# Kernel optimization log

Hardware: AMD Instinct MI355X
Metric: run time of the kernel (lower is better)

Reference implementation:

```python
import jax, jax.numpy as jnp
import numpy as np

EPS = np.finfo(np.float32).eps
X_DIM, H_DIM, Z_DIM = 256, 1024, 128
T, B = 128, 256

def _lin(key, fan_in, fan_out):
    k1, k2 = jax.random.split(key)
    lim = 1.0 / np.sqrt(fan_in)
    W = jax.random.uniform(k1, (fan_in, fan_out), jnp.float32, -lim, lim)
    b = jax.random.uniform(k2, (fan_out,), jnp.float32, -lim, lim)
    return W, b

def setup_inputs() -> dict:
    key = jax.random.key(0)
    ks = jax.random.split(key, 20)
    inp = {}
    inp['x'] = jax.random.normal(ks[0], (T, B, X_DIM), jnp.float32)
    inp['h'] = jnp.zeros((1, B, H_DIM), jnp.float32)
    inp['eps'] = jax.random.normal(ks[1], (T, B, Z_DIM), jnp.float32)
    inp['Wpx'], inp['bpx'] = _lin(ks[2], X_DIM, H_DIM)
    inp['Wpz'], inp['bpz'] = _lin(ks[3], Z_DIM, H_DIM)
    inp['Wenc'], inp['benc'] = _lin(ks[4], 2 * H_DIM, H_DIM)
    inp['Wem'], inp['bem'] = _lin(ks[5], H_DIM, Z_DIM)
    inp['Wes'], inp['bes'] = _lin(ks[6], H_DIM, Z_DIM)
    inp['Wpr'], inp['bpr'] = _lin(ks[7], H_DIM, H_DIM)
    inp['Wpm'], inp['bpm'] = _lin(ks[8], H_DIM, Z_DIM)
    inp['Wps'], inp['bps'] = _lin(ks[9], H_DIM, Z_DIM)
    inp['Wdec'], inp['bdec'] = _lin(ks[10], 2 * H_DIM, H_DIM)
    inp['Wdm'], inp['bdm'] = _lin(ks[11], H_DIM, X_DIM)
    inp['Wds'], inp['bds'] = _lin(ks[12], H_DIM, X_DIM)
    # GRU (pytorch layout): W_ih [3H, 2H], W_hh [3H, H]
    lim = 1.0 / np.sqrt(H_DIM)
    inp['W_ih'] = jax.random.uniform(ks[13], (3 * H_DIM, 2 * H_DIM), jnp.float32, -lim, lim)
    inp['W_hh'] = jax.random.uniform(ks[14], (3 * H_DIM, H_DIM), jnp.float32, -lim, lim)
    inp['b_ih'] = jax.random.uniform(ks[15], (3 * H_DIM,), jnp.float32, -lim, lim)
    inp['b_hh'] = jax.random.uniform(ks[16], (3 * H_DIM,), jnp.float32, -lim, lim)
    return inp

def reference(x, h, eps, Wpx, bpx, Wpz, bpz, Wenc, benc, Wem, bem, Wes, bes,
              Wpr, bpr, Wpm, bpm, Wps, bps, Wdec, bdec, Wdm, bdm, Wds, bds,
              W_ih, W_hh, b_ih, b_hh):
    relu = jax.nn.relu
    sp = jax.nn.softplus

    def gru_cell(inp, h_prev):
        gi = inp @ W_ih.T + b_ih          # [B, 3H]
        gh = h_prev @ W_hh.T + b_hh       # [B, 3H]
        i_r, i_z, i_n = jnp.split(gi, 3, axis=-1)
        h_r, h_z, h_n = jnp.split(gh, 3, axis=-1)
        r = jax.nn.sigmoid(i_r + h_r)
        u = jax.nn.sigmoid(i_z + h_z)
        n = jnp.tanh(i_n + r * h_n)
        return (1.0 - u) * n + u * h_prev

    def step(h_t, xe):
        x_t, eps_t = xe
        phi_x_t = relu(x_t @ Wpx + bpx)                               # [B,H]
        enc_t = relu(jnp.concatenate([phi_x_t, h_t], axis=1) @ Wenc + benc)
        enc_mean_t = enc_t @ Wem + bem
        enc_std_t = sp(enc_t @ Wes + bes)
        z_t = enc_mean_t + eps_t * enc_std_t                          # reparam
        phi_z_t = relu(z_t @ Wpz + bpz)
        prior_t = relu(h_t @ Wpr + bpr)
        prior_mean_t = prior_t @ Wpm + bpm
        prior_std_t = sp(prior_t @ Wps + bps)
        dec_t = relu(jnp.concatenate([phi_z_t, h_t], axis=1) @ Wdec + bdec)
        dec_mean_t = dec_t @ Wdm + bdm
        dec_std_t = sp(dec_t @ Wds + bds)
        h_next = gru_cell(jnp.concatenate([phi_x_t, phi_z_t], axis=1), h_t)
        kld_t = 0.5 * jnp.sum(2.0 * jnp.log(prior_std_t + EPS) - 2.0 * jnp.log(enc_std_t + EPS)
                              + (enc_std_t ** 2 + (enc_mean_t - prior_mean_t) ** 2) / prior_std_t ** 2 - 1.0)
        nll_t = jnp.sum(jnp.log(dec_std_t + EPS) + 0.5 * jnp.log(2.0 * jnp.pi)
                        + (x_t - dec_mean_t) ** 2 / (2.0 * dec_std_t ** 2))
        return h_next, (enc_mean_t, enc_std_t, dec_mean_t, dec_std_t, kld_t, nll_t)

    h0 = h[0]  # [B, H]
    _, (enc_means, enc_stds, dec_means, dec_stds, klds, nlls) = jax.lax.scan(step, h0, (x, eps))
    kld_loss = jnp.sum(klds)
    nll_loss = jnp.sum(nlls)
    return (kld_loss, nll_loss, enc_means, enc_stds, dec_means, dec_stds)
```

## Files before the change

### kernel.cpp

```cpp
#include <hip/hip_runtime.h>
#include <math.h>
#include <limits.h>

#define T_DIM 128
#define B_DIM 256
#define X_DIMC 256
#define H_DIMC 1024
#define Z_DIMC 128
#define EPSF 1.1920929e-07f
#define HALF_LOG_2PI 0.91893853320467274f
#define NBLK 768
#define NPB (NBLK / 64)
#define BARN ((66 + 64) * 32)

typedef float f32x4 __attribute__((ext_vector_type(4)));
typedef short bf16x8 __attribute__((ext_vector_type(8)));

struct Seg { int n_end; int kbeg; int kend; const float* bias; int act;
             float* of32; int ld32; short* ob16; int ld16; };
struct Segs { Seg s[4]; };

__host__ __device__ static inline Seg dseg(int n_end, int kbeg, int kend,
    const float* bias, int act, float* of32, int ld32, short* ob16, int ld16)
{
    Seg s; s.n_end = n_end; s.kbeg = kbeg; s.kend = kend; s.bias = bias;
    s.act = act; s.of32 = of32; s.ld32 = ld32; s.ob16 = ob16; s.ld16 = ld16;
    return s;
}
__host__ __device__ static inline Seg dsegend()
{ return dseg(INT_MAX, 0, 64, nullptr, 0, nullptr, 0, nullptr, 0); }

__device__ __forceinline__ short f2bf(float f) {
    unsigned u = __builtin_bit_cast(unsigned, f);
    u += 0x7fffu + ((u >> 16) & 1u);
    return (short)(u >> 16);
}
__device__ __forceinline__ float act_apply(float x, int act) {
    if (act == 1) return fmaxf(x, 0.f);
    if (act == 2) return x > 0.f ? x + log1pf(expf(-x)) : log1pf(expf(x));
    return x;
}
__device__ __forceinline__ void gload16(const short* g, short* l) {
    __builtin_amdgcn_global_load_lds(
        (const __attribute__((address_space(1))) void*)g,
        (__attribute__((address_space(3))) void*)l, 16, 0, 0);
}
__device__ __forceinline__ void gload16a(const short* g, short* l) {
    __builtin_amdgcn_global_load_lds(
        (const __attribute__((address_space(1))) void*)g,
        (__attribute__((address_space(3))) void*)l, 16, 0, 17);
}
__device__ __forceinline__ float ldf(const float* p) {
    return __hip_atomic_load(p, __ATOMIC_RELAXED, __HIP_MEMORY_SCOPE_AGENT);
}
__device__ __forceinline__ void stf(float* p, float v) {
    __hip_atomic_store(p, v, __ATOMIC_RELAXED, __HIP_MEMORY_SCOPE_AGENT);
}
__device__ __forceinline__ void sth(short* p, short v) {
    __hip_atomic_store(p, v, __ATOMIC_RELAXED, __HIP_MEMORY_SCOPE_AGENT);
}

__device__ __forceinline__ void gridbar(unsigned* bar, int phase) {
    __syncthreads();
    if (threadIdx.x == 0) {
        asm volatile("s_waitcnt vmcnt(0) lgkmcnt(0)" ::: "memory");
        const int leaf = blockIdx.x & 63;
        unsigned* leafc = bar + (leaf << 5);
        unsigned* rootc = bar + (64 << 5);
        unsigned* rgen  = bar + (65 << 5);
        unsigned* lgen  = bar + ((66 + leaf) << 5);
        unsigned old = __hip_atomic_fetch_add(leafc, 1u, __ATOMIC_RELAXED,
                                              __HIP_MEMORY_SCOPE_AGENT);
        if (((old + 1u) % (unsigned)NPB) == 0u) {
            unsigned r = __hip_atomic_fetch_add(rootc, 1u, __ATOMIC_RELAXED,
                                                __HIP_MEMORY_SCOPE_AGENT);
            if (((r + 1u) & 63u) == 0u)
                __hip_atomic_store(rgen, (r + 1u) >> 6, __ATOMIC_RELAXED,
                                   __HIP_MEMORY_SCOPE_AGENT);
            unsigned g; int it = 0;
            while ((int)(g = __hip_atomic_load(rgen, __ATOMIC_RELAXED,
                                               __HIP_MEMORY_SCOPE_AGENT)) < phase) {
                if (it < 4) { __builtin_amdgcn_s_sleep(1); ++it; }
                else        { __builtin_amdgcn_s_sleep(8); }
            }
            __hip_atomic_store(lgen, g, __ATOMIC_RELAXED,
                               __HIP_MEMORY_SCOPE_AGENT);
        } else {
            int it = 0;
            while ((int)__hip_atomic_load(lgen, __ATOMIC_RELAXED,
                                          __HIP_MEMORY_SCOPE_AGENT) < phase) {
                if (it < 4) { __builtin_amdgcn_s_sleep(1); ++it; }
                else        { __builtin_amdgcn_s_sleep(8); }
            }
        }
    }
    __syncthreads();
}

__device__ __forceinline__ void gemm_tile(
    short* __restrict__ smem, int bm0, int bn0,
    const short* __restrict__ A0, int lda0,
    const short* __restrict__ A1, int lda1,
    const short* __restrict__ A2, int lda2,
    int ks1, int ks2, int a0c,
    const short* __restrict__ BT, int ldb, const Segs& segs)
{
    short* As = smem;
    short* Bs = smem + 12288;
    const int tid = threadIdx.x, lane = tid & 63, wid = tid >> 6;
    __syncthreads();
    Seg sg; int n0;
    if      (bn0 < segs.s[0].n_end) { sg = segs.s[0]; n0 = 0; }
    else if (bn0 < segs.s[1].n_end) { sg = segs.s[1]; n0 = segs.s[0].n_end; }
    else if (bn0 < segs.s[2].n_end) { sg = segs.s[2]; n0 = segs.s[1].n_end; }
    else                            { sg = segs.s[3]; n0 = segs.s[2].n_end; }
    const int nit = (sg.kend - sg.kbeg) >> 5;
    const int row16 = lane >> 2;
    const int kc = ((lane & 3) ^ ((lane >> 3) & 3)) << 3;
    const int r0 = (wid << 4) + row16;

    auto srcA = [&](int gk) -> const short* {
        return (gk < ks1) ? A0 + (size_t)(bm0 + r0) * lda0 + gk
             : (gk < ks2) ? A1 + (size_t)(bm0 + r0) * lda1 + (gk - ks1)
                          : A2 + (size_t)(bm0 + r0) * lda2 + (gk - ks2);
    };
    auto stage = [&](int p, int it) {
        const int gk = sg.kbeg + (it << 5) + kc;
        short* dA = As + p * 2048 + (wid << 9);
        short* dB = Bs + p * 2048 + (wid << 9);
        const short* ga = srcA(gk);
        if (a0c && gk < ks1) gload16(ga, dA);
        else                 gload16a(ga, dA);
        gload16(BT + (size_t)(bn0 + r0) * ldb + gk, dB);
    };

    const int l15 = lane & 15, lg = lane >> 4;
    const int wm = (wid >> 1) << 5, wn = (wid & 1) << 5;
    const int co = (lg ^ ((l15 >> 1) & 3)) << 3;
    f32x4 acc[2][2] = {};

#pragma unroll
    for (int i = 0; i < 6; ++i) if (i < nit) stage(i, i);
    int p = 0;
    for (int it = 0; it < nit; ++it) {
        const int rem = nit - 1 - it;
        if      (rem >= 5) asm volatile("s_waitcnt vmcnt(10)" ::: "memory");
        else if (rem == 4) asm volatile("s_waitcnt vmcnt(8)" ::: "memory");
        else if (rem == 3) asm volatile("s_waitcnt vmcnt(6)" ::: "memory");
        else if (rem == 2) asm volatile("s_waitcnt vmcnt(4)" ::: "memory");
        else if (rem == 1) asm volatile("s_waitcnt vmcnt(2)" ::: "memory");
        else               asm volatile("s_waitcnt vmcnt(0)" ::: "memory");
        asm volatile("s_barrier" ::: "memory");
        const short* Ap = As + p * 2048;
        const short* Bp = Bs + p * 2048;
        bf16x8 a0 = *(const bf16x8*)(Ap + (wm + l15) * 32 + co);
        bf16x8 a1 = *(const bf16x8*)(Ap + (wm + 16 + l15) * 32 + co);
        bf16x8 b0 = *(const bf16x8*)(Bp + (wn + l15) * 32 + co);
        bf16x8 b1 = *(const bf16x8*)(Bp + (wn + 16 + l15) * 32 + co);
        acc[0][0] = __builtin_amdgcn_mfma_f32_16x16x32_bf16(a0, b0, acc[0][0], 0, 0, 0);
        acc[0][1] = __builtin_amdgcn_mfma_f32_16x16x32_bf16(a0, b1, acc[0][1], 0, 0, 0);
        acc[1][0] = __builtin_amdgcn_mfma_f32_16x16x32_bf16(a1, b0, acc[1][0], 0, 0, 0);
        acc[1][1] = __builtin_amdgcn_mfma_f32_16x16x32_bf16(a1, b1, acc[1][1], 0, 0, 0);
        if (rem >= 6) {
            asm volatile("s_waitcnt lgkmcnt(0)\n\ts_barrier" ::: "memory");
            stage(p, it + 6);
        }
        p = (p == 5) ? 0 : p + 1;
    }

#pragma unroll
    for (int j = 0; j < 2; ++j) {
        const int gn = bn0 + wn + (j << 4) + l15;
        const int cn = gn - n0;
        const float bv = sg.bias[cn];
#pragma unroll
        for (int i = 0; i < 2; ++i) {
            const int gm0 = bm0 + wm + (i << 4) + (lg << 2);
#pragma unroll
            for (int r = 0; r < 4; ++r) {
                float v = act_apply(acc[i][j][r] + bv, sg.act);
                if (sg.of32) stf(sg.of32 + (size_t)(gm0 + r) * sg.ld32 + cn, v);
                if (sg.ob16) sth(sg.ob16 + (size_t)(gm0 + r) * sg.ld16 + cn, f2bf(v));
            }
        }
    }
}

__device__ __forceinline__ void z_tile(
    short* __restrict__ smem, int bm0, int bn0,
    const float* __restrict__ zm, const float* __restrict__ zs,
    const float* __restrict__ ze,
    const short* __restrict__ BT, const float* __restrict__ bias,
    short* __restrict__ outb)
{
    short* Az = smem;
    short* Bz = smem + 64 * 136;
    const int tid = threadIdx.x, lane = tid & 63, wid = tid >> 6;
    __syncthreads();
    const int r = tid >> 2, c0i = (tid & 3) << 3;
#pragma unroll
    for (int s = 0; s < 4; ++s) {
        const int col = c0i + s * 32;
        const size_t base = (size_t)(bm0 + r) * 128 + col;
        short tmp[8];
#pragma unroll
        for (int q = 0; q < 8; ++q) {
            const float m = ldf(zm + base + q);
            const float sd = ldf(zs + base + q);
            const float e = ze[base + q];
            tmp[q] = f2bf(fmaf(e, sd, m));
        }
        *(bf16x8*)(Az + r * 136 + col) = *(bf16x8*)tmp;
        *(bf16x8*)(Bz + r * 136 + col) =
            *(const bf16x8*)(BT + (size_t)(bn0 + r) * 128 + col);
    }
    __syncthreads();
    const int l15 = lane & 15, lg = lane >> 4;
    const int wm = (wid >> 1) << 5, wn = (wid & 1) << 5;
    f32x4 acc[2][2] = {};
#pragma unroll
    for (int s = 0; s < 4; ++s) {
        bf16x8 af0 = *(const bf16x8*)(Az + (wm + l15) * 136 + (lg << 3) + s * 32);
        bf16x8 af1 = *(const bf16x8*)(Az + (wm + 16 + l15) * 136 + (lg << 3) + s * 32);
        bf16x8 bg0 = *(const bf16x8*)(Bz + (wn + l15) * 136 + (lg << 3) + s * 32);
        bf16x8 bg1 = *(const bf16x8*)(Bz + (wn + 16 + l15) * 136 + (lg << 3) + s * 32);
        acc[0][0] = __builtin_amdgcn_mfma_f32_16x16x32_bf16(af0, bg0, acc[0][0], 0, 0, 0);
        acc[0][1] = __builtin_amdgcn_mfma_f32_16x16x32_bf16(af0, bg1, acc[0][1], 0, 0, 0);
        acc[1][0] = __builtin_amdgcn_mfma_f32_16x16x32_bf16(af1, bg0, acc[1][0], 0, 0, 0);
        acc[1][1] = __builtin_amdgcn_mfma_f32_16x16x32_bf16(af1, bg1, acc[1][1], 0, 0, 0);
    }
#pragma unroll
    for (int j = 0; j < 2; ++j) {
        const int gn = bn0 + wn + (j << 4) + l15;
        const float bv = bias[gn];
#pragma unroll
        for (int i = 0; i < 2; ++i) {
            const int gm0 = bm0 + wm + (i << 4) + (lg << 2);
#pragma unroll
            for (int rr = 0; rr < 4; ++rr) {
                float v = fmaxf(acc[i][j][rr] + bv, 0.f);
                sth(outb + (size_t)(gm0 + rr) * 1024 + gn, f2bf(v));
            }
        }
    }
}

__device__ __forceinline__ void gru_unit(int uid, int tid,
    const float* __restrict__ gi, const float* __restrict__ gh,
    const float* __restrict__ h, float* __restrict__ hn, short* __restrict__ hnb)
{
    const int i = uid * 256 + tid;
    const int b = i >> 10, j = i & (H_DIMC - 1);
    const float* gib = gi + (size_t)b * 3 * H_DIMC;
    const float* ghb = gh + (size_t)b * 3 * H_DIMC;
    const float r = 1.f / (1.f + expf(-(ldf(gib + j) + ldf(ghb + j))));
    const float u = 1.f / (1.f + expf(-(ldf(gib + H_DIMC + j) + ldf(ghb + H_DIMC + j))));
    const float n = tanhf(ldf(gib + 2 * H_DIMC + j) + r * ldf(ghb + 2 * H_DIMC + j));
    const float v = (1.f - u) * n + u * ldf(h + i);
    stf(hn + i, v); sth(hnb + i, f2bf(v));
}

__device__ __forceinline__ void loss_unit(int uid, int tid,
    const float* __restrict__ em, const float* __restrict__ es,
    const float* __restrict__ pm, const float* __restrict__ ps,
    const float* __restrict__ xt, const float* __restrict__ dm,
    const float* __restrict__ ds, float* __restrict__ outp, float* sred)
{
    const int KB = (B_DIM * Z_DIMC) / 256;
    float v; int target;
    if (uid < KB) {
        const int i = uid * 256 + tid;
        const float esv = ldf(es + i), psv = ldf(ps + i);
        const float dmn = ldf(em + i) - ldf(pm + i);
        v = 0.5f * (2.f * logf(psv + EPSF) - 2.f * logf(esv + EPSF) +
                    (esv * esv + dmn * dmn) / (psv * psv) - 1.f);
        target = 0;
    } else {
        const int i = (uid - KB) * 256 + tid;
        const float d = ldf(ds + i);
        const float diff = xt[i] - ldf(dm + i);
        v = logf(d + EPSF) + HALF_LOG_2PI + diff * diff / (2.f * d * d);
        target = 1;
    }
    for (int o = 32; o > 0; o >>= 1) v += __shfl_down(v, o);
    if ((tid & 63) == 0) sred[tid >> 6] = v;
    __syncthreads();
    if (tid == 0) atomicAdd(outp + target, sred[0] + sred[1] + sred[2] + sred[3]);
    __syncthreads();
}

struct PP {
    const short* xb; const float* x; const float* eps;
    const short *WTpx, *WT1, *WT2, *WTpz, *WT4, *WT56;
    const float *bpx, *benc, *bpr, *bhh, *bem, *bes, *bpz, *bdec, *bih,
                *bpm, *bps, *bdm, *bds;
    float *hf0, *hf1; short *hb0, *hb1;
    short *enc_b, *prior_b, *phi_zb, *dec_b;
    short *phiXb, *phiXs;
    float *ghb, *gib, *pmb, *psb;
    float *kld, *em, *es, *dm, *ds;
    unsigned* bar; int big;
};

__global__ __launch_bounds__(256, 3) void vrnn_k(PP p)
{
    __shared__ short smem[24576];
    __shared__ float sred[4];
    const int G = gridDim.x, bid = blockIdx.x, tid = threadIdx.x;
    const int BIGK = 1 << 30;
    int ph = 0;

    Segs sx;
    sx.s[0] = dseg(1024, 0, 256, p.bpx, 1, nullptr, 0, p.big ? p.phiXb : p.phiXs, 1024);
    sx.s[1] = dsegend(); sx.s[2] = dsegend(); sx.s[3] = dsegend();

    if (p.big) {
        for (int u = bid; u < 512 * 16; u += G)
            gemm_tile(smem, (u & 511) << 6, (u >> 9) << 6,
                      p.xb, 256, p.xb, 256, p.xb, 256, BIGK, BIGK, 1,
                      p.WTpx, 256, sx);
        gridbar(p.bar, ++ph);
    }

    for (int t = 0; t < T_DIM; ++t) {
        float* hcur = (t & 1) ? p.hf1 : p.hf0;
        float* hnxt = (t & 1) ? p.hf0 : p.hf1;
        const short* hbc = (t & 1) ? p.hb1 : p.hb0;
        short* hbn = (t & 1) ? p.hb0 : p.hb1;
        const short* phiXt = p.big ? p.phiXb + (size_t)t * B_DIM * H_DIMC : p.phiXs;
        float* em_t = p.em + (size_t)t * B_DIM * Z_DIMC;
        float* es_t = p.es + (size_t)t * B_DIM * Z_DIMC;
        float* dm_t = p.dm + (size_t)t * B_DIM * X_DIMC;
        float* ds_t = p.ds + (size_t)t * B_DIM * X_DIMC;
        const float* eps_t = p.eps + (size_t)t * B_DIM * Z_DIMC;

        if (!p.big) {
            for (int u = bid; u < 64; u += G)
                gemm_tile(smem, (u & 3) << 6, (u >> 2) << 6,
                          p.xb + (size_t)t * B_DIM * X_DIMC, 256,
                          p.xb, 256, p.xb, 256, BIGK, BIGK, 1, p.WTpx, 256, sx);
            gridbar(p.bar, ++ph);
        }
        {
            Segs g1;
            g1.s[0] = dseg(1024, 0, 2048, p.benc, 1, nullptr, 0, p.enc_b, 1024);
            g1.s[1] = dseg(2048, 1024, 2048, p.bpr, 1, nullptr, 0, p.prior_b, 1024);
            g1.s[2] = dseg(5120, 1024, 2048, p.bhh, 0, p.ghb, 3 * H_DIMC, nullptr, 0);
            g1.s[3] = dsegend();
            const int tp = t - 1;
            const int nA = 320 + (t > 0 ? 384 : 0);
            for (int u = bid; u < nA; u += G) {
                if (u < 320)
                    gemm_tile(smem, (u & 3) << 6, (u >> 2) << 6,
                              phiXt, 1024, hbc, 1024, hbc, 1024, 1024, BIGK, 1,
                              p.WT1, 2048, g1);
                else
                    loss_unit(u - 320, tid,
                              p.em + (size_t)tp * B_DIM * Z_DIMC,
                              p.es + (size_t)tp * B_DIM * Z_DIMC,
                              p.pmb, p.psb,
                              p.x + (size_t)tp * B_DIM * X_DIMC,
                              p.dm + (size_t)tp * B_DIM * X_DIMC,
                              p.ds + (size_t)tp * B_DIM * X_DIMC,
                              p.kld, sred);
            }
            gridbar(p.bar, ++ph);
        }
        {
            Segs g2;
            g2.s[0] = dseg(128, 0, 1024, p.bem, 0, em_t, 128, nullptr, 0);
            g2.s[1] = dseg(256, 0, 1024, p.bes, 2, es_t, 128, nullptr, 0);
            g2.s[2] = dsegend(); g2.s[3] = dsegend();
            for (int u = bid; u < 16; u += G)
                gemm_tile(smem, (u & 3) << 6, (u >> 2) << 6,
                          p.enc_b, 1024, p.enc_b, 1024, p.enc_b, 1024, BIGK, BIGK, 0,
                          p.WT2, 1024, g2);
            gridbar(p.bar, ++ph);
        }
        for (int u = bid; u < 64; u += G)
            z_tile(smem, (u & 3) << 6, (u >> 2) << 6,
                   em_t, es_t, eps_t, p.WTpz, p.bpz, p.phi_zb);
        gridbar(p.bar, ++ph);
        {
            Segs g4;
            g4.s[0] = dseg(1024, 1024, 3072, p.bdec, 1, nullptr, 0, p.dec_b, 1024);
            g4.s[1] = dseg(4096, 0, 2048, p.bih, 0, p.gib, 3 * H_DIMC, nullptr, 0);
            g4.s[2] = dsegend(); g4.s[3] = dsegend();
            for (int u = bid; u < 256; u += G)
                gemm_tile(smem, (u & 3) << 6, (u >> 2) << 6,
                          phiXt, 1024, p.phi_zb, 1024, hbc, 1024, 1024, 2048, 1,
                          p.WT4, 3072, g4);
            gridbar(p.bar, ++ph);
        }
        {
            Segs g5;
            g5.s[0] = dseg(128, 0, 1024, p.bpm, 0, p.pmb, 128, nullptr, 0);
            g5.s[1] = dseg(256, 0, 1024, p.bps, 2, p.psb, 128, nullptr, 0);
            g5.s[2] = dseg(512, 1024, 2048, p.bdm, 0, dm_t, 256, nullptr, 0);
            g5.s[3] = dseg(768, 1024, 2048, p.bds, 2, ds_t, 256, nullptr, 0);
            for (int u = bid; u < 48 + 1024; u += G) {
                if (u < 48)
                    gemm_tile(smem, (u & 3) << 6, (u >> 2) << 6,
                              p.prior_b, 1024, p.dec_b, 1024, p.dec_b, 1024,
                              1024, BIGK, 0, p.WT56, 2048, g5);
                else
                    gru_unit(u - 48, tid, p.gib, p.ghb, hcur, hnxt, hbn);
            }
            gridbar(p.bar, ++ph);
        }
    }
    {
        const int tp = T_DIM - 1;
        for (int u = bid; u < 384; u += G)
            loss_unit(u, tid,
                      p.em + (size_t)tp * B_DIM * Z_DIMC,
                      p.es + (size_t)tp * B_DIM * Z_DIMC,
                      p.pmb, p.psb,
                      p.x + (size_t)tp * B_DIM * X_DIMC,
                      p.dm + (size_t)tp * B_DIM * X_DIMC,
                      p.ds + (size_t)tp * B_DIM * X_DIMC,
                      p.kld, sred);
    }
}

__global__ void packT_k(const float* __restrict__ src, int ldsr,
                        short* __restrict__ dst, int ldd, int n0, int k0)
{
    __shared__ float tile[32][33];
    const int bx = blockIdx.x * 32, by = blockIdx.y * 32;
    const int tx = threadIdx.x, ty = threadIdx.y;
    for (int i = ty; i < 32; i += 8)
        tile[i][tx] = src[(size_t)(by + i) * ldsr + bx + tx];
    __syncthreads();
    for (int i = ty; i < 32; i += 8)
        dst[(size_t)(n0 + bx + i) * ldd + k0 + by + tx] = f2bf(tile[tx][i]);
}

__global__ void packD_k(const float* __restrict__ src, int ldsr,
                        short* __restrict__ dst, int ldd, int n0, int k0, int kr)
{
    const int idx = blockIdx.x * 256 + threadIdx.x;
    const int n = idx / kr, k = idx % kr;
    dst[(size_t)(n0 + n) * ldd + k0 + k] = f2bf(src[(size_t)n * ldsr + k]);
}

__global__ void cvtx_k(const float* __restrict__ x, short* __restrict__ xb)
{
    const int i = blockIdx.x * 256 + threadIdx.x;
    float4 v = ((const float4*)x)[i];
    short4 s;
    s.x = f2bf(v.x); s.y = f2bf(v.y); s.z = f2bf(v.z); s.w = f2bf(v.w);
    ((short4*)xb)[i] = s;
}

__global__ void hinit_k(const float* __restrict__ h0, float* __restrict__ hf,
                        short* __restrict__ hb)
{
    const int i = blockIdx.x * 256 + threadIdx.x;
    const float v = h0[i];
    hf[i] = v; hb[i] = f2bf(v);
}

__global__ void init_k(unsigned* bar, float* kn)
{
    for (int i = threadIdx.x; i < BARN; i += 256) bar[i] = 0u;
    if (threadIdx.x < 2) kn[threadIdx.x] = 0.f;
}

extern "C" void kernel_launch(void* const* d_in, const int* in_sizes, int n_in,
                              void* d_out_v, int out_size, void* d_ws, size_t ws_size,
                              hipStream_t stream)
{
    (void)in_sizes; (void)n_in; (void)out_size;
    const float* x    = (const float*)d_in[0];
    const float* h0   = (const float*)d_in[1];
    const float* eps  = (const float*)d_in[2];
    const float* Wpx  = (const float*)d_in[3];
    const float* bpx  = (const float*)d_in[4];
    const float* Wpz  = (const float*)d_in[5];
    const float* bpz  = (const float*)d_in[6];
    const float* Wenc = (const float*)d_in[7];
    const float* benc = (const float*)d_in[8];
    const float* Wem  = (const float*)d_in[9];
    const float* bem  = (const float*)d_in[10];
    const float* Wes  = (const float*)d_in[11];
    const float* bes  = (const float*)d_in[12];
    const float* Wpr  = (const float*)d_in[13];
    const float* bpr  = (const float*)d_in[14];
    const float* Wpm  = (const float*)d_in[15];
    const float* bpm  = (const float*)d_in[16];
    const float* Wps  = (const float*)d_in[17];
    const float* bps  = (const float*)d_in[18];
    const float* Wdec = (const float*)d_in[19];
    const float* bdec = (const float*)d_in[20];
    const float* Wdm  = (const float*)d_in[21];
    const float* bdm  = (const float*)d_in[22];
    const float* Wds  = (const float*)d_in[23];
    const float* bds  = (const float*)d_in[24];
    const float* W_ih = (const float*)d_in[25];
    const float* W_hh = (const float*)d_in[26];
    const float* b_ih = (const float*)d_in[27];
    const float* b_hh = (const float*)d_in[28];

    float* out = (float*)d_out_v;

    char* wsb = (char*)d_ws;
    size_t off = 0;
    auto takeB = [&](size_t bytes) {
        char* p = wsb + off; off += (bytes + 255) & ~(size_t)255; return p;
    };
    short* WTpx = (short*)takeB((size_t)1024 * 256 * 2);
    short* WT1  = (short*)takeB((size_t)5120 * 2048 * 2);
    short* WT2  = (short*)takeB((size_t)256 * 1024 * 2);
    short* WTpz = (short*)takeB((size_t)1024 * 128 * 2);
    short* WT4  = (short*)takeB((size_t)4096 * 3072 * 2);
    short* WT56 = (short*)takeB((size_t)768 * 2048 * 2);
    short* xb   = (short*)takeB((size_t)T_DIM * B_DIM * X_DIMC * 2);
    float* hf0  = (float*)takeB((size_t)B_DIM * H_DIMC * 4);
    float* hf1  = (float*)takeB((size_t)B_DIM * H_DIMC * 4);
    short* hb0  = (short*)takeB((size_t)B_DIM * H_DIMC * 2);
    short* hb1  = (short*)takeB((size_t)B_DIM * H_DIMC * 2);
    short* enc_b   = (short*)takeB((size_t)B_DIM * H_DIMC * 2);
    short* prior_b = (short*)takeB((size_t)B_DIM * H_DIMC * 2);
    short* phi_zb  = (short*)takeB((size_t)B_DIM * H_DIMC * 2);
    short* dec_b   = (short*)takeB((size_t)B_DIM * H_DIMC * 2);
    float* ghb_ = (float*)takeB((size_t)B_DIM * 3 * H_DIMC * 4);
    float* gib_ = (float*)takeB((size_t)B_DIM * 3 * H_DIMC * 4);
    float* pmb  = (float*)takeB((size_t)B_DIM * Z_DIMC * 4);
    float* psb  = (float*)takeB((size_t)B_DIM * Z_DIMC * 4);
    unsigned* bar = (unsigned*)takeB((size_t)BARN * 4);
    const size_t phiXb_bytes = (size_t)T_DIM * B_DIM * H_DIMC * 2;
    const bool big = (off + phiXb_bytes) <= ws_size;
    short* phiXb = big ? (short*)takeB(phiXb_bytes) : nullptr;
    short* phiXs = big ? nullptr : (short*)takeB((size_t)B_DIM * H_DIMC * 2);

    const dim3 tb(256), pt(32, 8);

    packT_k<<<dim3(32, 8), pt, 0, stream>>>(Wpx, 1024, WTpx, 256, 0, 0);
    packT_k<<<dim3(32, 64), pt, 0, stream>>>(Wenc, 1024, WT1, 2048, 0, 0);
    packT_k<<<dim3(32, 32), pt, 0, stream>>>(Wpr, 1024, WT1, 2048, 1024, 1024);
    packD_k<<<dim3(3072 * 1024 / 256), tb, 0, stream>>>(W_hh, 1024, WT1, 2048, 2048, 1024, 1024);
    packT_k<<<dim3(4, 32), pt, 0, stream>>>(Wem, 128, WT2, 1024, 0, 0);
    packT_k<<<dim3(4, 32), pt, 0, stream>>>(Wes, 128, WT2, 1024, 128, 0);
    packT_k<<<dim3(32, 4), pt, 0, stream>>>(Wpz, 1024, WTpz, 128, 0, 0);
    packT_k<<<dim3(32, 64), pt, 0, stream>>>(Wdec, 1024, WT4, 3072, 0, 1024);
    packD_k<<<dim3(3072 * 2048 / 256), tb, 0, stream>>>(W_ih, 2048, WT4, 3072, 1024, 0, 2048);
    packT_k<<<dim3(4, 32), pt, 0, stream>>>(Wpm, 128, WT56, 2048, 0, 0);
    packT_k<<<dim3(4, 32), pt, 0, stream>>>(Wps, 128, WT56, 2048, 128, 0);
    packT_k<<<dim3(8, 32), pt, 0, stream>>>(Wdm, 256, WT56, 2048, 256, 1024);
    packT_k<<<dim3(8, 32), pt, 0, stream>>>(Wds, 256, WT56, 2048, 512, 1024);

    cvtx_k<<<dim3((size_t)T_DIM * B_DIM * X_DIMC / 4 / 256), tb, 0, stream>>>(x, xb);
    hinit_k<<<dim3(B_DIM * H_DIMC / 256), tb, 0, stream>>>(h0, hf0, hb0);
    init_k<<<1, 256, 0, stream>>>(bar, out);

    PP p;
    p.xb = xb; p.x = x; p.eps = eps;
    p.WTpx = WTpx; p.WT1 = WT1; p.WT2 = WT2; p.WTpz = WTpz; p.WT4 = WT4; p.WT56 = WT56;
    p.bpx = bpx; p.benc = benc; p.bpr = bpr; p.bhh = b_hh; p.bem = bem; p.bes = bes;
    p.bpz = bpz; p.bdec = bdec; p.bih = b_ih; p.bpm = bpm; p.bps = bps;
    p.bdm = bdm; p.bds = bds;
    p.hf0 = hf0; p.hf1 = hf1; p.hb0 = hb0; p.hb1 = hb1;
    p.enc_b = enc_b; p.prior_b = prior_b; p.phi_zb = phi_zb; p.dec_b = dec_b;
    p.phiXb = phiXb; p.phiXs = phiXs;
    p.ghb = ghb_; p.gib = gib_; p.pmb = pmb; p.psb = psb;
    p.kld = out; p.em = out + 2;
    p.es = p.em + (size_t)T_DIM * B_DIM * Z_DIMC;
    p.dm = p.es + (size_t)T_DIM * B_DIM * Z_DIMC;
    p.ds = p.dm + (size_t)T_DIM * B_DIM * X_DIMC;
    p.bar = bar; p.big = big ? 1 : 0;

    vrnn_k<<<dim3(NBLK), tb, 0, stream>>>(p);
}
```

Baseline: 15.27 ms.

## Split persistent grid into two independent batch-half groups with separate barriers

Splits the 768-block persistent kernel into two groups of 384 blocks. Each group handles 128 batch rows and syncs on its own hierarchical grid barrier. Because the batch rows are independent through the recurrence, each barrier now waits on half as many blocks, which should cut barrier latency per phase. The cost is half the tiles per group per phase, so small GEMM phases leave even more blocks idle, and weight reads are duplicated across the groups.

Result: faster. 14.71 ms (-3.7%).

```diff
diff --git a/kernel.cpp b/kernel.cpp
--- a/kernel.cpp
+++ b/kernel.cpp
@@ -10,7 +10,8 @@
 #define EPSF 1.1920929e-07f
 #define HALF_LOG_2PI 0.91893853320467274f
 #define NBLK 768
-#define NPB (NBLK / 64)
+#define GBLK 384
+#define NPB (GBLK / 64)
 #define BARN ((66 + 64) * 32)
 
 typedef float f32x4 __attribute__((ext_vector_type(4)));
@@ -60,11 +61,11 @@
     __hip_atomic_store(p, v, __ATOMIC_RELAXED, __HIP_MEMORY_SCOPE_AGENT);
 }
 
-__device__ __forceinline__ void gridbar(unsigned* bar, int phase) {
+__device__ __forceinline__ void gridbar(unsigned* bar, int phase, int lbid) {
     __syncthreads();
     if (threadIdx.x == 0) {
         asm volatile("s_waitcnt vmcnt(0) lgkmcnt(0)" ::: "memory");
-        const int leaf = blockIdx.x & 63;
+        const int leaf = lbid & 63;
         unsigned* leafc = bar + (leaf << 5);
         unsigned* rootc = bar + (64 << 5);
         unsigned* rgen  = bar + (65 << 5);
@@ -245,11 +246,11 @@
     }
 }
 
-__device__ __forceinline__ void gru_unit(int uid, int tid,
+__device__ __forceinline__ void gru_unit(int uid, int tid, int rb,
     const float* __restrict__ gi, const float* __restrict__ gh,
     const float* __restrict__ h, float* __restrict__ hn, short* __restrict__ hnb)
 {
-    const int i = uid * 256 + tid;
+    const int i = rb * H_DIMC + uid * 256 + tid;
     const int b = i >> 10, j = i & (H_DIMC - 1);
     const float* gib = gi + (size_t)b * 3 * H_DIMC;
     const float* ghb = gh + (size_t)b * 3 * H_DIMC;
@@ -266,7 +267,7 @@
     const float* __restrict__ xt, const float* __restrict__ dm,
     const float* __restrict__ ds, float* __restrict__ outp, float* sred)
 {
-    const int KB = (B_DIM * Z_DIMC) / 256;
+    const int KB = 64;
     float v; int target;
     if (uid < KB) {
         const int i = uid * 256 + tid;
@@ -306,7 +307,10 @@
 {
     __shared__ short smem[24576];
     __shared__ float sred[4];
-    const int G = gridDim.x, bid = blockIdx.x, tid = threadIdx.x;
+    const int bid = blockIdx.x, tid = threadIdx.x;
+    const int g = bid / GBLK, lbid = bid % GBLK;
+    const int rb = g << 7;
+    unsigned* bar = p.bar + (size_t)g * BARN;
     const int BIGK = 1 << 30;
     int ph = 0;
 
@@ -315,11 +319,14 @@
     sx.s[1] = dsegend(); sx.s[2] = dsegend(); sx.s[3] = dsegend();
 
     if (p.big) {
-        for (int u = bid; u < 512 * 16; u += G)
-            gemm_tile(smem, (u & 511) << 6, (u >> 9) << 6,
+        for (int u = lbid; u < 256 * 16; u += GBLK) {
+            const int mt = u & 255;
+            const int bm0 = ((mt >> 1) << 8) + rb + ((mt & 1) << 6);
+            gemm_tile(smem, bm0, (u >> 8) << 6,
                       p.xb, 256, p.xb, 256, p.xb, 256, BIGK, BIGK, 1,
                       p.WTpx, 256, sx);
-        gridbar(p.bar, ++ph);
+        }
+        gridbar(bar, ++ph, lbid);
     }
 
     for (int t = 0; t < T_DIM; ++t) {
@@ -335,11 +342,11 @@
         const float* eps_t = p.eps + (size_t)t * B_DIM * Z_DIMC;
 
         if (!p.big) {
-            for (int u = bid; u < 64; u += G)
-                gemm_tile(smem, (u & 3) << 6, (u >> 2) << 6,
+            for (int u = lbid; u < 32; u += GBLK)
+                gemm_tile(smem, (size_t)t * 0 + rb + ((u & 1) << 6), (u >> 1) << 6,
                           p.xb + (size_t)t * B_DIM * X_DIMC, 256,
                           p.xb, 256, p.xb, 256, BIGK, BIGK, 1, p.WTpx, 256, sx);
-            gridbar(p.bar, ++ph);
+            gridbar(bar, ++ph, lbid);
         }
         {
             Segs g1;
@@ -348,49 +355,49 @@
             g1.s[2] = dseg(5120, 1024, 2048, p.bhh, 0, p.ghb, 3 * H_DIMC, nullptr, 0);
             g1.s[3] = dsegend();
             const int tp = t - 1;
-            const int nA = 320 + (t > 0 ? 384 : 0);
-            for (int u = bid; u < nA; u += G) {
-                if (u < 320)
-                    gemm_tile(smem, (u & 3) << 6, (u >> 2) << 6,
+            const int nA = 160 + (t > 0 ? 192 : 0);
+            for (int u = lbid; u < nA; u += GBLK) {
+                if (u < 160)
+                    gemm_tile(smem, rb + ((u & 1) << 6), (u >> 1) << 6,
                               phiXt, 1024, hbc, 1024, hbc, 1024, 1024, BIGK, 1,
                               p.WT1, 2048, g1);
                 else
-                    loss_unit(u - 320, tid,
-                              p.em + (size_t)tp * B_DIM * Z_DIMC,
-                              p.es + (size_t)tp * B_DIM * Z_DIMC,
-                              p.pmb, p.psb,
-                              p.x + (size_t)tp * B_DIM * X_DIMC,
-                              p.dm + (size_t)tp * B_DIM * X_DIMC,
-                              p.ds + (size_t)tp * B_DIM * X_DIMC,
+                    loss_unit(u - 160, tid,
+                              p.em + (size_t)tp * B_DIM * Z_DIMC + (size_t)rb * Z_DIMC,
+                              p.es + (size_t)tp * B_DIM * Z_DIMC + (size_t)rb * Z_DIMC,
+                              p.pmb + (size_t)rb * Z_DIMC, p.psb + (size_t)rb * Z_DIMC,
+                              p.x + (size_t)tp * B_DIM * X_DIMC + (size_t)rb * X_DIMC,
+                              p.dm + (size_t)tp * B_DIM * X_DIMC + (size_t)rb * X_DIMC,
+                              p.ds + (size_t)tp * B_DIM * X_DIMC + (size_t)rb * X_DIMC,
                               p.kld, sred);
             }
-            gridbar(p.bar, ++ph);
+            gridbar(bar, ++ph, lbid);
         }
         {
             Segs g2;
             g2.s[0] = dseg(128, 0, 1024, p.bem, 0, em_t, 128, nullptr, 0);
             g2.s[1] = dseg(256, 0, 1024, p.bes, 2, es_t, 128, nullptr, 0);
             g2.s[2] = dsegend(); g2.s[3] = dsegend();
-            for (int u = bid; u < 16; u += G)
-                gemm_tile(smem, (u & 3) << 6, (u >> 2) << 6,
+            for (int u = lbid; u < 8; u += GBLK)
+                gemm_tile(smem, rb + ((u & 1) << 6), (u >> 1) << 6,
                           p.enc_b, 1024, p.enc_b, 1024, p.enc_b, 1024, BIGK, BIGK, 0,
                           p.WT2, 1024, g2);
-            gridbar(p.bar, ++ph);
-        }
-        for (int u = bid; u < 64; u += G)
-            z_tile(smem, (u & 3) << 6, (u >> 2) << 6,
+            gridbar(bar, ++ph, lbid);
+        }
+        for (int u = lbid; u < 32; u += GBLK)
+            z_tile(smem, rb + ((u & 1) << 6), (u >> 1) << 6,
                    em_t, es_t, eps_t, p.WTpz, p.bpz, p.phi_zb);
-        gridbar(p.bar, ++ph);
+        gridbar(bar, ++ph, lbid);
         {
             Segs g4;
             g4.s[0] = dseg(1024, 1024, 3072, p.bdec, 1, nullptr, 0, p.dec_b, 1024);
             g4.s[1] = dseg(4096, 0, 2048, p.bih, 0, p.gib, 3 * H_DIMC, nullptr, 0);
             g4.s[2] = dsegend(); g4.s[3] = dsegend();
-            for (int u = bid; u < 256; u += G)
-                gemm_tile(smem, (u & 3) << 6, (u >> 2) << 6,
+            for (int u = lbid; u < 128; u += GBLK)
+                gemm_tile(smem, rb + ((u & 1) << 6), (u >> 1) << 6,
                           phiXt, 1024, p.phi_zb, 1024, hbc, 1024, 1024, 2048, 1,
                           p.WT4, 3072, g4);
-            gridbar(p.bar, ++ph);
+            gridbar(bar, ++ph, lbid);
         }
         {
             Segs g5;
@@ -398,27 +405,27 @@
             g5.s[1] = dseg(256, 0, 1024, p.bps, 2, p.psb, 128, nullptr, 0);
             g5.s[2] = dseg(512, 1024, 2048, p.bdm, 0, dm_t, 256, nullptr, 0);
             g5.s[3] = dseg(768, 1024, 2048, p.bds, 2, ds_t, 256, nullptr, 0);
-            for (int u = bid; u < 48 + 1024; u += G) {
-                if (u < 48)
-                    gemm_tile(smem, (u & 3) << 6, (u >> 2) << 6,
+            for (int u = lbid; u < 24 + 512; u += GBLK) {
+                if (u < 24)
+                    gemm_tile(smem, rb + ((u & 1) << 6), (u >> 1) << 6,
                               p.prior_b, 1024, p.dec_b, 1024, p.dec_b, 1024,
                               1024, BIGK, 0, p.WT56, 2048, g5);
                 else
-                    gru_unit(u - 48, tid, p.gib, p.ghb, hcur, hnxt, hbn);
+                    gru_unit(u - 24, tid, rb, p.gib, p.ghb, hcur, hnxt, hbn);
             }
-            gridbar(p.bar, ++ph);
+            gridbar(bar, ++ph, lbid);
         }
     }
     {
         const int tp = T_DIM - 1;
-        for (int u = bid; u < 384; u += G)
+        for (int u = lbid; u < 192; u += GBLK)
             loss_unit(u, tid,
-                      p.em + (size_t)tp * B_DIM * Z_DIMC,
-                      p.es + (size_t)tp * B_DIM * Z_DIMC,
-                      p.pmb, p.psb,
-                      p.x + (size_t)tp * B_DIM * X_DIMC,
-                      p.dm + (size_t)tp * B_DIM * X_DIMC,
-                      p.ds + (size_t)tp * B_DIM * X_DIMC,
+                      p.em + (size_t)tp * B_DIM * Z_DIMC + (size_t)rb * Z_DIMC,
+                      p.es + (size_t)tp * B_DIM * Z_DIMC + (size_t)rb * Z_DIMC,
+                      p.pmb + (size_t)rb * Z_DIMC, p.psb + (size_t)rb * Z_DIMC,
+                      p.x + (size_t)tp * B_DIM * X_DIMC + (size_t)rb * X_DIMC,
+                      p.dm + (size_t)tp * B_DIM * X_DIMC + (size_t)rb * X_DIMC,
+                      p.ds + (size_t)tp * B_DIM * X_DIMC + (size_t)rb * X_DIMC,
                       p.kld, sred);
     }
 }
@@ -463,7 +470,7 @@
 
 __global__ void init_k(unsigned* bar, float* kn)
 {
-    for (int i = threadIdx.x; i < BARN; i += 256) bar[i] = 0u;
+    for (int i = threadIdx.x; i < 2 * BARN; i += 256) bar[i] = 0u;
     if (threadIdx.x < 2) kn[threadIdx.x] = 0.f;
 }
 
@@ -528,7 +535,7 @@
     float* gib_ = (float*)takeB((size_t)B_DIM * 3 * H_DIMC * 4);
     float* pmb  = (float*)takeB((size_t)B_DIM * Z_DIMC * 4);
     float* psb  = (float*)takeB((size_t)B_DIM * Z_DIMC * 4);
-    unsigned* bar = (unsigned*)takeB((size_t)BARN * 4);
+    unsigned* bar = (unsigned*)takeB((size_t)2 * BARN * 4);
     const size_t phiXb_bytes = (size_t)T_DIM * B_DIM * H_DIMC * 2;
     const bool big = (off + phiXb_bytes) <= ws_size;
     short* phiXb = big ? (short*)takeB(phiXb_bytes) : nullptr;
```
